# Kernel tuning notes

Measured on AMD Instinct MI355X. Metric: run time of the kernel, lower is better.

Reference implementation:

```python
import jax, jax.numpy as jnp
import numpy as np

N = 100000      # spots (nodes)
E = 1600000     # directed edges
D_IN = 1000     # genes
ALPHA = 0.9
BN_EPS = 1e-3   # BatchNorm(momentum=0.01, eps=0.001), eval mode


def _bn(x, g, b, m, v):
    # eval-mode batchnorm with running stats
    return (x - m) * jax.lax.rsqrt(v + BN_EPS) * g + b


def _gcn(h, row, col, w, b):
    # PyG GCNConv: h' = D^-1/2 (A + I) D^-1/2 (h W) + b
    n = h.shape[0]
    h = h @ w
    ones = jnp.ones((row.shape[0],), h.dtype)
    deg = jnp.ones((n,), h.dtype).at[col].add(ones)  # degree incl. self-loop
    dinv = jax.lax.rsqrt(deg)
    msg = h[row] * (dinv[row] * dinv[col])[:, None]   # gather + edge norm
    agg = jnp.zeros_like(h).at[col].add(msg)          # scatter-add
    agg = agg + h * (1.0 / deg)[:, None]              # self-loop term
    return agg + b


def setup_inputs() -> dict:
    key = jax.random.key(0)
    ks = iter(jax.random.split(key, 48))
    f32 = jnp.float32

    def glorot(shape):
        return jax.random.normal(next(ks), shape, f32) * np.float32(1.0 / np.sqrt(shape[0]))

    def bnp(n):
        g = jax.random.uniform(next(ks), (n,), f32, 0.9, 1.1)
        b = jax.random.normal(next(ks), (n,), f32) * 0.1
        m = jax.random.normal(next(ks), (n,), f32) * 0.1
        v = jax.random.uniform(next(ks), (n,), f32, 0.5, 1.5)
        return g, b, m, v

    inp = {}
    inp['x'] = jax.random.normal(next(ks), (N, D_IN), f32)
    inp['edge_index'] = jax.random.randint(next(ks), (2, E), 0, N, jnp.int64)
    # encoder L0: 1000 -> 256
    inp['enc0_w'] = glorot((D_IN, 256)); inp['enc0_b'] = jnp.zeros((256,), f32)
    inp['enc0_g'], inp['enc0_bb'], inp['enc0_m'], inp['enc0_v'] = bnp(256)
    # encoder L1: 256 -> 64
    inp['enc1_w'] = glorot((256, 64)); inp['enc1_b'] = jnp.zeros((64,), f32)
    inp['enc1_g'], inp['enc1_bb'], inp['enc1_m'], inp['enc1_v'] = bnp(64)
    # GCN: 64 -> 128 (conv_hidden[0]*2)
    inp['conv_w'] = glorot((64, 128)); inp['conv_b'] = jnp.zeros((128,), f32)
    inp['conv_g'], inp['conv_bb'], inp['conv_m'], inp['conv_v'] = bnp(128)
    # GCN mean / logvar heads: 128 -> 16
    inp['mean_w'] = glorot((128, 16)); inp['mean_b'] = jnp.zeros((16,), f32)
    inp['logvar_w'] = glorot((128, 16)); inp['logvar_b'] = jnp.zeros((16,), f32)
    # decoder L0: 80 -> 64
    inp['dec0_w'] = glorot((80, 64)); inp['dec0_b'] = jnp.zeros((64,), f32)
    inp['dec0_g'], inp['dec0_bb'], inp['dec0_m'], inp['dec0_v'] = bnp(64)
    # decoder L1: 64 -> 1000
    inp['dec1_w'] = glorot((64, D_IN)); inp['dec1_b'] = jnp.zeros((D_IN,), f32)
    # cluster layer [15, 80]
    inp['cluster'] = jax.random.normal(next(ks), (15, 80), f32) * np.float32(np.sqrt(2.0 / (15 + 80)))
    return inp


def reference(x, edge_index, enc0_w, enc0_b, enc0_g, enc0_bb, enc0_m, enc0_v,
              enc1_w, enc1_b, enc1_g, enc1_bb, enc1_m, enc1_v,
              conv_w, conv_b, conv_g, conv_bb, conv_m, conv_v,
              mean_w, mean_b, logvar_w, logvar_b,
              dec0_w, dec0_b, dec0_g, dec0_bb, dec0_m, dec0_v,
              dec1_w, dec1_b, cluster):
    row, col = edge_index[0], edge_index[1]
    # linear encoder (Linear + BN(eval) + ELU; dropout off in eval)
    h = jax.nn.elu(_bn(x @ enc0_w + enc0_b, enc0_g, enc0_bb, enc0_m, enc0_v))
    feat_x = jax.nn.elu(_bn(h @ enc1_w + enc1_b, enc1_g, enc1_bb, enc1_m, enc1_v))
    # graph encoder
    c = jax.nn.relu(_bn(_gcn(feat_x, row, col, conv_w, conv_b), conv_g, conv_bb, conv_m, conv_v))
    mu = _gcn(c, row, col, mean_w, mean_b)
    logvar = _gcn(c, row, col, logvar_w, logvar_b)
    gnn_z = mu  # reparameterize in eval mode returns mu
    z = jnp.concatenate([feat_x, gnn_z], axis=1)  # [N, 80]
    # decoder
    d = jax.nn.elu(_bn(z @ dec0_w + dec0_b, dec0_g, dec0_bb, dec0_m, dec0_v))
    de_feat = d @ dec1_w + dec1_b
    # student-t cluster soft assignment (||z-c||^2 via expansion, no [N,K,80] tensor)
    dist = jnp.maximum(jnp.sum(z * z, 1, keepdims=True)
                       + jnp.sum(cluster * cluster, 1)[None, :]
                       - 2.0 * (z @ cluster.T), 0.0)
    q = 1.0 / (1.0 + dist / ALPHA + 1e-8)
    q = q ** ((ALPHA + 1.0) / 2.0)
    q = q / jnp.sum(q, 1, keepdims=True)
    return (z, mu, logvar, de_feat, q, feat_x, gnn_z)
```

## Files before the change

### kernel.cpp

```cpp
#include <hip/hip_runtime.h>
#include <hip/hip_bf16.h>

#define NN 100000
#define NE 1600000
#define DIN 1000
#define BN_EPS 1e-3f
#define NB 391

#define OZ  ((size_t)0)
#define OMU ((size_t)NN*80)
#define OLV ((size_t)NN*96)
#define ODE ((size_t)NN*112)
#define OQ  ((size_t)NN*1112)
#define OFX ((size_t)NN*1127)
#define OGZ ((size_t)NN*1191)

typedef __attribute__((ext_vector_type(8))) short short8v;
typedef __attribute__((ext_vector_type(4))) short short4v;
typedef __attribute__((ext_vector_type(4))) float f32x4;

__device__ __forceinline__ float elu_f(float x) { return x > 0.f ? x : expf(x) - 1.f; }

__device__ __forceinline__ short f2bf(float f) {
    union { float f; unsigned u; } c; c.f = f;
    unsigned r = c.u + 0x7fffu + ((c.u >> 16) & 1u);
    return (short)(r >> 16);
}
__device__ __forceinline__ float b2f(short s) {
    union { unsigned u; float f; } c; c.u = ((unsigned)(unsigned short)s) << 16; return c.f;
}
__device__ __forceinline__ float b2f_lo(unsigned p) {
    union { unsigned u; float f; } c; c.u = p << 16; return c.f;
}
__device__ __forceinline__ float b2f_hi(unsigned p) {
    union { unsigned u; float f; } c; c.u = p & 0xffff0000u; return c.f;
}

__device__ __forceinline__ int edge_at(const void* ei, int is64, size_t idx) {
    if (is64) return (int)((const long long*)ei)[idx];
    return ((const int*)ei)[idx];
}

__global__ __launch_bounds__(256) void k_deg_init(const int* __restrict__ ei,
                                                  float* __restrict__ deg, int* __restrict__ flag) {
    const int i = blockIdx.x * 256 + threadIdx.x;
    if (i < NN) deg[i] = 1.0f;
    if (blockIdx.x == 0) {
        __shared__ int nz;
        if (threadIdx.x == 0) nz = 0;
        __syncthreads();
        for (int j = threadIdx.x; j < 2048; j += 256)
            if (ei[2 * j + 1] != 0) nz = 1;
        __syncthreads();
        if (threadIdx.x == 0) flag[0] = (nz == 0) ? 1 : 0;
    }
}

__global__ __launch_bounds__(256) void k_deg_accum(const void* __restrict__ ei, const int* __restrict__ flag,
                                                   float* __restrict__ deg) {
    const int is64 = flag[0];
    int e = blockIdx.x * 256 + threadIdx.x;
    if (e < NE) atomicAdd(&deg[edge_at(ei, is64, (size_t)NE + e)], 1.0f);
}

__global__ __launch_bounds__(256) void k_scan1(const float* __restrict__ deg, int* __restrict__ off,
                                               int* __restrict__ bsum, int* __restrict__ cursor) {
    __shared__ int s[256];
    const int t = threadIdx.x;
    const int i = blockIdx.x * 256 + t;
    const int vv = (i < NN) ? ((int)deg[i]) - 1 : 0;
    if (i < NN) cursor[i] = 0;
    s[t] = vv;
    __syncthreads();
    for (int d = 1; d < 256; d <<= 1) {
        const int u = (t >= d) ? s[t - d] : 0;
        __syncthreads();
        s[t] += u;
        __syncthreads();
    }
    if (i < NN) off[i] = s[t] - vv;
    if (t == 255) bsum[blockIdx.x] = s[t];
}

__global__ __launch_bounds__(512) void k_scan2(int* __restrict__ bsum) {
    __shared__ int s[512];
    const int t = threadIdx.x;
    const int vv = (t < NB) ? bsum[t] : 0;
    s[t] = vv;
    __syncthreads();
    for (int d = 1; d < 512; d <<= 1) {
        const int u = (t >= d) ? s[t - d] : 0;
        __syncthreads();
        s[t] += u;
        __syncthreads();
    }
    if (t < NB) bsum[t] = s[t] - vv;
}

__global__ __launch_bounds__(256) void k_scan3(int* __restrict__ off, const int* __restrict__ bsum) {
    const int i = blockIdx.x * 256 + threadIdx.x;
    if (i < NN) off[i] += bsum[blockIdx.x];
}

__global__ __launch_bounds__(256) void k_fill(const void* __restrict__ ei, const int* __restrict__ flag,
                                              const float* __restrict__ deg, const int* __restrict__ off,
                                              int* __restrict__ cursor, int2* __restrict__ csr_e) {
    const int is64 = flag[0];
    const int e = blockIdx.x * 256 + threadIdx.x;
    if (e >= NE) return;
    const int r = edge_at(ei, is64, e);
    const int c = edge_at(ei, is64, (size_t)NE + e);
    const float w = rsqrtf(deg[r]) * rsqrtf(deg[c]);
    const int p = atomicAdd(&cursor[c], 1);
    csr_e[off[c] + p] = make_int2(r, __float_as_int(w));
}

__global__ __launch_bounds__(256) void k_wts(const float* __restrict__ w0, short* __restrict__ wt,
                                             const float* __restrict__ w1, short* __restrict__ wt2) {
    const int bid = blockIdx.x;
    if (bid < 1024) {
        const int tid = bid * 256 + threadIdx.x;
        const int c = tid >> 10;
        const int k = tid & 1023;
        wt[((size_t)(k >> 3) * 256 + c) * 8 + (k & 7)] = (k < DIN) ? f2bf(w0[(size_t)k * 256 + c]) : (short)0;
    } else {
        const int tid = (bid - 1024) * 256 + threadIdx.x;
        const int c = tid >> 6;
        const int k = tid & 63;
        wt2[(size_t)c * 64 + k] = (c < DIN) ? f2bf(w1[(size_t)k * DIN + c]) : (short)0;
    }
}

__global__ __launch_bounds__(512, 2) void k_enc0_mfma(
    const float* __restrict__ x, const short* __restrict__ wt, const float* __restrict__ bias,
    const float* __restrict__ g, const float* __restrict__ bb,
    const float* __restrict__ m, const float* __restrict__ v,
    short* __restrict__ h1bf)
{
    __shared__ short smem[24576];
    const int t = threadIdx.x;
    const int lane = t & 63;
    const int wave = t >> 6;
    const int wm = (wave >> 2) * 64;
    const int wn = (wave & 3) * 64;
    const int row0 = blockIdx.x * 128;

    f32x4 acc[4][4];
    #pragma unroll
    for (int mi = 0; mi < 4; ++mi)
        #pragma unroll
        for (int ni = 0; ni < 4; ++ni)
            acc[mi][ni] = (f32x4){0.f, 0.f, 0.f, 0.f};

    const int kq = t & 7;
    const int rA0 = t >> 3;
    const int rA1 = rA0 + 64;
    const int gr0 = (row0 + rA0 < NN) ? (row0 + rA0) : (NN - 1);
    const int gr1 = (row0 + rA1 < NN) ? (row0 + rA1) : (NN - 1);
    const float* xb0 = x + (size_t)gr0 * DIN;
    const float* xb1 = x + (size_t)gr1 * DIN;
    const size_t aoff0 = (((kq >> 1) * 128) + rA0) * 8 + (kq & 1) * 4;
    const size_t aoff1 = (((kq >> 1) * 128) + rA1) * 8 + (kq & 1) * 4;

    const int colB = t & 255;
    const int kcB0 = t >> 8;
    const int kcB1 = 2 + (t >> 8);
    const size_t boff0 = ((size_t)kcB0 * 256 + colB) * 8;
    const size_t boff1 = ((size_t)kcB1 * 256 + colB) * 8;

    const int kc = lane >> 4;
    const int lr = lane & 15;

    {
        const float4 f0 = *reinterpret_cast<const float4*>(xb0 + kq * 4);
        const float4 f1 = *reinterpret_cast<const float4*>(xb1 + kq * 4);
        short4v p0, p1;
        p0[0] = f2bf(f0.x); p0[1] = f2bf(f0.y); p0[2] = f2bf(f0.z); p0[3] = f2bf(f0.w);
        p1[0] = f2bf(f1.x); p1[1] = f2bf(f1.y); p1[2] = f2bf(f1.z); p1[3] = f2bf(f1.w);
        *reinterpret_cast<short4v*>(&smem[aoff0]) = p0;
        *reinterpret_cast<short4v*>(&smem[aoff1]) = p1;
        *reinterpret_cast<short8v*>(&smem[8192 + boff0]) =
            *reinterpret_cast<const short8v*>(&wt[((size_t)kcB0 * 256 + colB) * 8]);
        *reinterpret_cast<short8v*>(&smem[8192 + boff1]) =
            *reinterpret_cast<const short8v*>(&wt[((size_t)kcB1 * 256 + colB) * 8]);
    }
    __syncthreads();

    for (int ks = 0; ks < 32; ++ks) {
        const int cur = ks & 1;
        const int nxt = cur ^ 1;
        const int abase_c = cur * 4096;
        const int bbase_c = 8192 + cur * 8192;
        float4 pf0, pf1;
        short8v wb0, wb1;
        const bool have_next = (ks + 1) < 32;
        bool next_a_ok = false;
        if (have_next) {
            const int kb2 = (ks + 1) * 32 + kq * 4;
            next_a_ok = (kb2 + 4 <= DIN);
            const int ko = next_a_ok ? kb2 : 0;
            pf0 = *reinterpret_cast<const float4*>(xb0 + ko);
            pf1 = *reinterpret_cast<const float4*>(xb1 + ko);
            const int gbase = (ks + 1) * 4;
            wb0 = *reinterpret_cast<const short8v*>(&wt[((size_t)(gbase + kcB0) * 256 + colB) * 8]);
            wb1 = *reinterpret_cast<const short8v*>(&wt[((size_t)(gbase + kcB1) * 256 + colB) * 8]);
        }
        short8v a[4], b[4];
        #pragma unroll
        for (int mi = 0; mi < 4; ++mi)
            a[mi] = *reinterpret_cast<const short8v*>(&smem[abase_c + ((size_t)kc * 128 + wm + mi * 16 + lr) * 8]);
        #pragma unroll
        for (int ni = 0; ni < 4; ++ni)
            b[ni] = *reinterpret_cast<const short8v*>(&smem[bbase_c + ((size_t)kc * 256 + wn + ni * 16 + lr) * 8]);
        #pragma unroll
        for (int mi = 0; mi < 4; ++mi)
            #pragma unroll
            for (int ni = 0; ni < 4; ++ni)
                acc[mi][ni] = __builtin_amdgcn_mfma_f32_16x16x32_bf16(a[mi], b[ni], acc[mi][ni], 0, 0, 0);
        if (have_next) {
            const int abase_n = nxt * 4096;
            const int bbase_n = 8192 + nxt * 8192;
            short4v p0, p1;
            if (next_a_ok) {
                p0[0] = f2bf(pf0.x); p0[1] = f2bf(pf0.y); p0[2] = f2bf(pf0.z); p0[3] = f2bf(pf0.w);
                p1[0] = f2bf(pf1.x); p1[1] = f2bf(pf1.y); p1[2] = f2bf(pf1.z); p1[3] = f2bf(pf1.w);
            } else {
                p0 = (short4v){0, 0, 0, 0};
                p1 = (short4v){0, 0, 0, 0};
            }
            *reinterpret_cast<short4v*>(&smem[abase_n + aoff0]) = p0;
            *reinterpret_cast<short4v*>(&smem[abase_n + aoff1]) = p1;
            *reinterpret_cast<short8v*>(&smem[bbase_n + boff0]) = wb0;
            *reinterpret_cast<short8v*>(&smem[bbase_n + boff1]) = wb1;
        }
        __syncthreads();
    }

    float sc[4], sh[4];
    #pragma unroll
    for (int ni = 0; ni < 4; ++ni) {
        const int col = wn + ni * 16 + lr;
        const float s = rsqrtf(v[col] + BN_EPS) * g[col];
        sc[ni] = s;
        sh[ni] = (bias[col] - m[col]) * s + bb[col];
    }
    #pragma unroll
    for (int p = 0; p < 2; ++p) {
        __syncthreads();
        if ((wave >> 2) == p) {
            #pragma unroll
            for (int mi = 0; mi < 4; ++mi) {
                #pragma unroll
                for (int j = 0; j < 4; ++j) {
                    const int lrow = mi * 16 + (lane >> 4) * 4 + j;
                    #pragma unroll
                    for (int ni = 0; ni < 4; ++ni) {
                        const float y = acc[mi][ni][j] * sc[ni] + sh[ni];
                        smem[lrow * 256 + wn + ni * 16 + lr] = f2bf(elu_f(y));
                    }
                }
            }
        }
        __syncthreads();
        for (int idx = t; idx < 2048; idx += 512) {
            const int r = idx >> 5;
            const int c8 = (idx & 31) * 8;
            const int row = row0 + p * 64 + r;
            if (row < NN)
                *reinterpret_cast<short8v*>(&h1bf[(size_t)row * 256 + c8]) =
                    *reinterpret_cast<const short8v*>(&smem[r * 256 + c8]);
        }
    }
}

__global__ __launch_bounds__(256) void k_enc1(
    const short* __restrict__ h1bf, const float* __restrict__ w, const float* __restrict__ bias,
    const float* __restrict__ g, const float* __restrict__ bb,
    const float* __restrict__ m, const float* __restrict__ v,
    float* __restrict__ feat, short* __restrict__ featbf, float* __restrict__ out)
{
    __shared__ short hs[32 * 256];
    const int t = threadIdx.x;
    const int row0 = blockIdx.x * 32;
    const int j0 = t & 31;
    const int r0 = (t >> 5) * 4;
    float acc[4][2] = {};
    for (int idx = t; idx < 1024; idx += 256) {
        const int r = idx >> 5, c8 = idx & 31;
        *reinterpret_cast<short8v*>(&hs[r * 256 + c8 * 8]) =
            *reinterpret_cast<const short8v*>(&h1bf[(size_t)(row0 + r) * 256 + c8 * 8]);
    }
    __syncthreads();
    #pragma unroll 1
    for (int k = 0; k < 256; k += 8) {
        float wv[8][2];
        #pragma unroll
        for (int kk = 0; kk < 8; ++kk) {
            wv[kk][0] = w[(k + kk) * 64 + j0];
            wv[kk][1] = w[(k + kk) * 64 + j0 + 32];
        }
        #pragma unroll
        for (int r = 0; r < 4; ++r) {
            const short8v hv = *reinterpret_cast<const short8v*>(&hs[(r0 + r) * 256 + k]);
            #pragma unroll
            for (int kk = 0; kk < 8; ++kk) {
                const float xa = b2f(hv[kk]);
                acc[r][0] = fmaf(xa, wv[kk][0], acc[r][0]);
                acc[r][1] = fmaf(xa, wv[kk][1], acc[r][1]);
            }
        }
    }
    #pragma unroll
    for (int c = 0; c < 2; ++c) {
        const int j = j0 + 32 * c;
        const float sc = rsqrtf(v[j] + BN_EPS) * g[j];
        const float sh = (bias[j] - m[j]) * sc + bb[j];
        #pragma unroll
        for (int r = 0; r < 4; ++r) {
            const size_t rowi = row0 + r0 + r;
            const float y = elu_f(acc[r][c] * sc + sh);
            feat[rowi * 64 + j] = y;
            featbf[rowi * 64 + j] = f2bf(y);
            out[OFX + rowi * 64 + j] = y;
            out[OZ + rowi * 80 + j] = y;
        }
    }
}

__global__ __launch_bounds__(256) void k_feat_gather(
    const unsigned* __restrict__ featp, const float* __restrict__ deg,
    const int* __restrict__ off, const int2* __restrict__ csr_e,
    float* __restrict__ aggF)
{
    const int t = threadIdx.x;
    const int node = blockIdx.x * 8 + (t >> 5);
    const int lane = t & 31;
    const float dg = deg[node];
    const float dinv = 1.0f / dg;
    const unsigned ps = featp[(size_t)node * 32 + lane];
    float a0 = b2f_lo(ps) * dinv;
    float a1 = b2f_hi(ps) * dinv;
    const int beg = off[node];
    const int end = beg + ((int)dg - 1);
    for (int s = beg; s < end; ++s) {
        const int2 e = csr_e[s];
        const float w = __int_as_float(e.y);
        const unsigned p = featp[(size_t)e.x * 32 + lane];
        a0 = fmaf(b2f_lo(p), w, a0);
        a1 = fmaf(b2f_hi(p), w, a1);
    }
    float2 o; o.x = a0; o.y = a1;
    *reinterpret_cast<float2*>(&aggF[(size_t)node * 64 + lane * 2]) = o;
}

__global__ __launch_bounds__(256) void k_conv_mlp_proj(
    const float* __restrict__ aggF, const float* __restrict__ w, const float* __restrict__ cb,
    const float* __restrict__ g, const float* __restrict__ bb,
    const float* __restrict__ m, const float* __restrict__ v,
    const float* __restrict__ mw, const float* __restrict__ lw,
    short* __restrict__ m2bf)
{
    __shared__ float fs[32 * 64];
    __shared__ float cs[32 * 128];
    const int t = threadIdx.x;
    const int row0 = blockIdx.x * 32;
    {
        const int j0 = t & 63;
        const int r0 = (t >> 6) * 8;
        float acc[8][2] = {};
        for (int idx = t; idx < 512; idx += 256) {
            const int r = idx >> 4, c4 = idx & 15;
            *reinterpret_cast<float4*>(&fs[r * 64 + c4 * 4]) =
                *reinterpret_cast<const float4*>(&aggF[(size_t)(row0 + r) * 64 + c4 * 4]);
        }
        __syncthreads();
        #pragma unroll 1
        for (int k = 0; k < 64; k += 4) {
            float wv[4][2];
            #pragma unroll
            for (int kk = 0; kk < 4; ++kk) {
                wv[kk][0] = w[(k + kk) * 128 + j0];
                wv[kk][1] = w[(k + kk) * 128 + j0 + 64];
            }
            #pragma unroll
            for (int r = 0; r < 8; ++r) {
                const float4 xv = *reinterpret_cast<const float4*>(&fs[(r0 + r) * 64 + k]);
                const float xa[4] = {xv.x, xv.y, xv.z, xv.w};
                #pragma unroll
                for (int kk = 0; kk < 4; ++kk) {
                    acc[r][0] = fmaf(xa[kk], wv[kk][0], acc[r][0]);
                    acc[r][1] = fmaf(xa[kk], wv[kk][1], acc[r][1]);
                }
            }
        }
        #pragma unroll
        for (int c = 0; c < 2; ++c) {
            const int j = j0 + 64 * c;
            const float sc = rsqrtf(v[j] + BN_EPS) * g[j];
            const float sh = bb[j] - m[j] * sc;
            const float cbj = cb[j];
            #pragma unroll
            for (int r = 0; r < 8; ++r) {
                const float val = acc[r][c] + cbj;
                cs[(r0 + r) * 128 + j] = fmaxf(fmaf(val, sc, sh), 0.f);
            }
        }
    }
    __syncthreads();
    {
        const int j0 = t & 15;
        const int r0 = (t >> 4) * 2;
        float acc[2][2] = {};
        #pragma unroll 1
        for (int k = 0; k < 128; k += 4) {
            float wv[4][2];
            #pragma unroll
            for (int kk = 0; kk < 4; ++kk) {
                wv[kk][0] = mw[(k + kk) * 16 + j0];
                wv[kk][1] = lw[(k + kk) * 16 + j0];
            }
            #pragma unroll
            for (int r = 0; r < 2; ++r) {
                const float4 xv = *reinterpret_cast<const float4*>(&cs[(r0 + r) * 128 + k]);
                const float xa[4] = {xv.x, xv.y, xv.z, xv.w};
                #pragma unroll
                for (int kk = 0; kk < 4; ++kk) {
                    acc[r][0] = fmaf(xa[kk], wv[kk][0], acc[r][0]);
                    acc[r][1] = fmaf(xa[kk], wv[kk][1], acc[r][1]);
                }
            }
        }
        #pragma unroll
        for (int r = 0; r < 2; ++r) {
            const size_t rowi = row0 + r0 + r;
            m2bf[rowi * 32 + j0] = f2bf(acc[r][0]);
            m2bf[rowi * 32 + 16 + j0] = f2bf(acc[r][1]);
        }
    }
}

__global__ __launch_bounds__(256) void k_mlp_gather(
    const unsigned* __restrict__ m2p, const float* __restrict__ deg,
    const int* __restrict__ off, const int2* __restrict__ csr_e,
    const float* __restrict__ mb, const float* __restrict__ lb,
    float* __restrict__ agg2)
{
    const int t = threadIdx.x;
    const int node = blockIdx.x * 16 + (t >> 4);
    const int lane = t & 15;
    const int f0 = lane * 2, f1 = lane * 2 + 1;
    const float dg = deg[node];
    const float dinv = 1.0f / dg;
    const float b0 = (f0 < 16) ? mb[f0] : lb[f0 - 16];
    const float b1 = (f1 < 16) ? mb[f1] : lb[f1 - 16];
    const unsigned ps = m2p[(size_t)node * 16 + lane];
    float a0 = fmaf(b2f_lo(ps), dinv, b0);
    float a1 = fmaf(b2f_hi(ps), dinv, b1);
    const int beg = off[node];
    const int end = beg + ((int)dg - 1);
    for (int s = beg; s < end; ++s) {
        const int2 e = csr_e[s];
        const float w = __int_as_float(e.y);
        const unsigned p = m2p[(size_t)e.x * 16 + lane];
        a0 = fmaf(b2f_lo(p), w, a0);
        a1 = fmaf(b2f_hi(p), w, a1);
    }
    float2 o; o.x = a0; o.y = a1;
    *reinterpret_cast<float2*>(&agg2[(size_t)node * 32 + lane * 2]) = o;
}

__global__ __launch_bounds__(256) void k_final_pre(
    const float* __restrict__ feat, const float* __restrict__ agg2,
    const float* __restrict__ d0w, const float* __restrict__ d0b,
    const float* __restrict__ g, const float* __restrict__ bb,
    const float* __restrict__ m, const float* __restrict__ v,
    const float* __restrict__ cluster,
    short* __restrict__ d0bf,
    float* __restrict__ out)
{
    __shared__ float zs[8][80];
    __shared__ float qs[8][15];
    const int t = threadIdx.x;
    const int row0 = blockIdx.x * 8;

    for (int idx = t; idx < 512; idx += 256) {
        const int r = idx >> 6, k = idx & 63;
        zs[r][k] = feat[(size_t)(row0 + r) * 64 + k];
    }
    if (t < 128) {
        const int r = t >> 4, k = t & 15;
        const size_t rowi = row0 + r;
        const float muv = agg2[rowi * 32 + k];
        const float lv = agg2[rowi * 32 + 16 + k];
        zs[r][64 + k] = muv;
        out[OMU + rowi * 16 + k] = muv;
        out[OGZ + rowi * 16 + k] = muv;
        out[OZ + rowi * 80 + 64 + k] = muv;
        out[OLV + rowi * 16 + k] = lv;
    }
    __syncthreads();

    for (int idx = t; idx < 512; idx += 256) {
        const int r = idx >> 6, n = idx & 63;
        float acc = 0.f;
        #pragma unroll
        for (int k = 0; k < 80; k += 4) {
            const float4 zv = *reinterpret_cast<const float4*>(&zs[r][k]);
            acc = fmaf(zv.x, d0w[(k + 0) * 64 + n], acc);
            acc = fmaf(zv.y, d0w[(k + 1) * 64 + n], acc);
            acc = fmaf(zv.z, d0w[(k + 2) * 64 + n], acc);
            acc = fmaf(zv.w, d0w[(k + 3) * 64 + n], acc);
        }
        acc += d0b[n];
        const float sc = rsqrtf(v[n] + BN_EPS) * g[n];
        const float y = elu_f((acc - m[n]) * sc + bb[n]);
        d0bf[(size_t)(row0 + r) * 64 + n] = f2bf(y);
    }

    if (t < 120) {
        const int r = t / 15, c = t % 15;
        float zz = 0.f, cc = 0.f, dot = 0.f;
        #pragma unroll 1
        for (int k = 0; k < 80; ++k) {
            const float zv = zs[r][k];
            const float cv = cluster[c * 80 + k];
            zz = fmaf(zv, zv, zz);
            cc = fmaf(cv, cv, cc);
            dot = fmaf(zv, cv, dot);
        }
        const float dist = fmaxf(zz + cc - 2.f * dot, 0.f);
        qs[r][c] = powf(1.0f / (1.0f + dist / 0.9f + 1e-8f), 0.95f);
    }
    __syncthreads();
    if (t < 120) {
        const int r = t / 15, c = t % 15;
        float s = 0.f;
        #pragma unroll
        for (int c2 = 0; c2 < 15; ++c2) s += qs[r][c2];
        out[OQ + (size_t)(row0 + r) * 15 + c] = qs[r][c] / s;
    }
}

__global__ __launch_bounds__(256) void k_dec1_mfma(
    const short* __restrict__ d0bf, const short* __restrict__ wt2,
    const float* __restrict__ d1b, float* __restrict__ out)
{
    __shared__ float ots[128 * 128];
    const int t = threadIdx.x;
    const int lane = t & 63;
    const int wave = t >> 6;
    const int wm = (wave >> 1) * 64;
    const int wn = (wave & 1) * 64;
    const int row0 = blockIdx.x * 128;
    const int col0 = blockIdx.y * 128;
    const int kc = lane >> 4;
    const int lr = lane & 15;

    f32x4 acc[4][4];
    #pragma unroll
    for (int mi = 0; mi < 4; ++mi)
        #pragma unroll
        for (int ni = 0; ni < 4; ++ni)
            acc[mi][ni] = (f32x4){0.f, 0.f, 0.f, 0.f};

    #pragma unroll
    for (int ks = 0; ks < 2; ++ks) {
        const int k0 = ks * 32 + kc * 8;
        short8v a[4], b[4];
        #pragma unroll
        for (int mi = 0; mi < 4; ++mi) {
            const int row = row0 + wm + mi * 16 + lr;
            if (row < NN)
                a[mi] = *reinterpret_cast<const short8v*>(&d0bf[(size_t)row * 64 + k0]);
            else
                a[mi] = (short8v){0, 0, 0, 0, 0, 0, 0, 0};
        }
        #pragma unroll
        for (int ni = 0; ni < 4; ++ni) {
            const int col = col0 + wn + ni * 16 + lr;
            b[ni] = *reinterpret_cast<const short8v*>(&wt2[(size_t)col * 64 + k0]);
        }
        #pragma unroll
        for (int mi = 0; mi < 4; ++mi)
            #pragma unroll
            for (int ni = 0; ni < 4; ++ni)
                acc[mi][ni] = __builtin_amdgcn_mfma_f32_16x16x32_bf16(a[mi], b[ni], acc[mi][ni], 0, 0, 0);
    }

    #pragma unroll
    for (int ni = 0; ni < 4; ++ni) {
        const int lcol = wn + ni * 16 + lr;
        const int gcol = col0 + lcol;
        const float bv = d1b[(gcol < DIN) ? gcol : (DIN - 1)];
        #pragma unroll
        for (int mi = 0; mi < 4; ++mi) {
            #pragma unroll
            for (int j = 0; j < 4; ++j) {
                const int lrow = wm + mi * 16 + (lane >> 4) * 4 + j;
                ots[lrow * 128 + lcol] = acc[mi][ni][j] + bv;
            }
        }
    }
    __syncthreads();

    for (int idx = t; idx < 128 * 32; idx += 256) {
        const int r = idx >> 5;
        const int c4 = (idx & 31) * 4;
        const int row = row0 + r;
        const int col = col0 + c4;
        if (row < NN && col < DIN) {
            const float4 val = *reinterpret_cast<const float4*>(&ots[r * 128 + c4]);
            *reinterpret_cast<float4*>(&out[ODE + (size_t)row * DIN + col]) = val;
        }
    }
}

extern "C" void kernel_launch(void* const* d_in, const int* in_sizes, int n_in,
                              void* d_out, int out_size, void* d_ws, size_t ws_size,
                              hipStream_t stream)
{
    const float* x       = (const float*)d_in[0];
    const void*  ei      = d_in[1];
    const float* enc0_w  = (const float*)d_in[2];
    const float* enc0_b  = (const float*)d_in[3];
    const float* enc0_g  = (const float*)d_in[4];
    const float* enc0_bb = (const float*)d_in[5];
    const float* enc0_m  = (const float*)d_in[6];
    const float* enc0_v  = (const float*)d_in[7];
    const float* enc1_w  = (const float*)d_in[8];
    const float* enc1_b  = (const float*)d_in[9];
    const float* enc1_g  = (const float*)d_in[10];
    const float* enc1_bb = (const float*)d_in[11];
    const float* enc1_m  = (const float*)d_in[12];
    const float* enc1_v  = (const float*)d_in[13];
    const float* conv_w  = (const float*)d_in[14];
    const float* conv_b  = (const float*)d_in[15];
    const float* conv_g  = (const float*)d_in[16];
    const float* conv_bb = (const float*)d_in[17];
    const float* conv_m  = (const float*)d_in[18];
    const float* conv_v  = (const float*)d_in[19];
    const float* mean_w  = (const float*)d_in[20];
    const float* mean_b  = (const float*)d_in[21];
    const float* logvar_w = (const float*)d_in[22];
    const float* logvar_b = (const float*)d_in[23];
    const float* dec0_w  = (const float*)d_in[24];
    const float* dec0_b  = (const float*)d_in[25];
    const float* dec0_g  = (const float*)d_in[26];
    const float* dec0_bb = (const float*)d_in[27];
    const float* dec0_m  = (const float*)d_in[28];
    const float* dec0_v  = (const float*)d_in[29];
    const float* dec1_w  = (const float*)d_in[30];
    const float* dec1_b  = (const float*)d_in[31];
    const float* cluster = (const float*)d_in[32];

    float* ws = (float*)d_ws;
    float* deg  = ws;
    float* feat = ws + NN;
    float* A    = ws + (size_t)65 * NN;
    size_t base = (size_t)321 * NN;
    int*   off     = (int*)(ws + base);
    int*   cursor  = (int*)(ws + base + NN);
    int*   bsum    = (int*)(ws + base + 2 * (size_t)NN);
    int2*  csr_e   = (int2*)(ws + base + 2 * (size_t)NN + 512);
    short* wt      = (short*)(ws + base + 2 * (size_t)NN + 512 + 2 * (size_t)NE);
    short* wt2     = wt + 262144;
    int*   flag    = (int*)(ws + base + 2 * (size_t)NN + 512 + 2 * (size_t)NE + 131072 + 32768);

    short* h1bf   = (short*)A;
    short* featbf = (short*)(A + (size_t)128 * NN);
    float* aggF   = A;
    short* m2bf   = (short*)(A + (size_t)128 * NN);
    float* agg2   = A + (size_t)32 * NN;
    short* d0bf   = (short*)(A + (size_t)64 * NN);

    float* out = (float*)d_out;

    k_deg_init<<<NB, 256, 0, stream>>>((const int*)ei, deg, flag);
    k_deg_accum<<<NE / 256, 256, 0, stream>>>(ei, flag, deg);

    k_scan1<<<NB, 256, 0, stream>>>(deg, off, bsum, cursor);
    k_scan2<<<1, 512, 0, stream>>>(bsum);
    k_scan3<<<NB, 256, 0, stream>>>(off, bsum);
    k_fill<<<NE / 256, 256, 0, stream>>>(ei, flag, deg, off, cursor, csr_e);

    k_wts<<<1280, 256, 0, stream>>>(enc0_w, wt, dec1_w, wt2);
    k_enc0_mfma<<<(NN + 127) / 128, 512, 0, stream>>>(x, wt, enc0_b, enc0_g, enc0_bb, enc0_m, enc0_v, h1bf);

    k_enc1<<<NN / 32, 256, 0, stream>>>(h1bf, enc1_w, enc1_b, enc1_g, enc1_bb, enc1_m, enc1_v,
                                        feat, featbf, out);

    k_feat_gather<<<NN / 8, 256, 0, stream>>>((const unsigned*)featbf, deg, off, csr_e, aggF);
    k_conv_mlp_proj<<<NN / 32, 256, 0, stream>>>(aggF, conv_w, conv_b,
                                                 conv_g, conv_bb, conv_m, conv_v,
                                                 mean_w, logvar_w, m2bf);

    k_mlp_gather<<<NN / 16, 256, 0, stream>>>((const unsigned*)m2bf, deg, off, csr_e,
                                              mean_b, logvar_b, agg2);

    k_final_pre<<<NN / 8, 256, 0, stream>>>(feat, agg2, dec0_w, dec0_b, dec0_g, dec0_bb, dec0_m, dec0_v,
                                            cluster, d0bf, out);
    {
        dim3 grid((NN + 127) / 128, 8);
        k_dec1_mfma<<<grid, 256, 0, stream>>>(d0bf, wt2, dec1_b, out);
    }
}
```

Measured before the change: 969.4 us.

## Factor GCN edge normalization into source/destination scaling and unroll gathers

Instead of storing a per-edge weight dinv[r]*dinv[c] in the CSR, source features are pre-scaled by rsqrt(deg) when written in bf16 and the gathered sum is scaled by the destination's rsqrt(deg). The CSR shrinks from int2 to int, which halves edge-list traffic, and the fill kernel no longer reads deg. The gather loops are unrolled by four with independent accumulators so more loads are in flight. Scaling before bf16 rounding slightly changes numerics, and the self-loop term now comes out as rsq*rsq*h, equal to h/deg.

Result: faster. 903.8 us (median of 2 runs) (-6.8%).

```diff
diff --git a/kernel.cpp b/kernel.cpp
--- a/kernel.cpp
+++ b/kernel.cpp
@@ -103,16 +103,15 @@
 }
 
 __global__ __launch_bounds__(256) void k_fill(const void* __restrict__ ei, const int* __restrict__ flag,
-                                              const float* __restrict__ deg, const int* __restrict__ off,
-                                              int* __restrict__ cursor, int2* __restrict__ csr_e) {
+                                              const int* __restrict__ off,
+                                              int* __restrict__ cursor, int* __restrict__ csr_src) {
     const int is64 = flag[0];
     const int e = blockIdx.x * 256 + threadIdx.x;
     if (e >= NE) return;
     const int r = edge_at(ei, is64, e);
     const int c = edge_at(ei, is64, (size_t)NE + e);
-    const float w = rsqrtf(deg[r]) * rsqrtf(deg[c]);
     const int p = atomicAdd(&cursor[c], 1);
-    csr_e[off[c] + p] = make_int2(r, __float_as_int(w));
+    csr_src[off[c] + p] = r;
 }
 
 __global__ __launch_bounds__(256) void k_wts(const float* __restrict__ w0, short* __restrict__ wt,
@@ -277,6 +276,7 @@
     const short* __restrict__ h1bf, const float* __restrict__ w, const float* __restrict__ bias,
     const float* __restrict__ g, const float* __restrict__ bb,
     const float* __restrict__ m, const float* __restrict__ v,
+    const float* __restrict__ deg,
     float* __restrict__ feat, short* __restrict__ featbf, float* __restrict__ out)
 {
     __shared__ short hs[32 * 256];
@@ -319,8 +319,9 @@
         for (int r = 0; r < 4; ++r) {
             const size_t rowi = row0 + r0 + r;
             const float y = elu_f(acc[r][c] * sc + sh);
+            const float rsq = rsqrtf(deg[rowi]);
             feat[rowi * 64 + j] = y;
-            featbf[rowi * 64 + j] = f2bf(y);
+            featbf[rowi * 64 + j] = f2bf(y * rsq);
             out[OFX + rowi * 64 + j] = y;
             out[OZ + rowi * 80 + j] = y;
         }
@@ -329,27 +330,37 @@
 
 __global__ __launch_bounds__(256) void k_feat_gather(
     const unsigned* __restrict__ featp, const float* __restrict__ deg,
-    const int* __restrict__ off, const int2* __restrict__ csr_e,
+    const int* __restrict__ off, const int* __restrict__ csr_src,
     float* __restrict__ aggF)
 {
     const int t = threadIdx.x;
     const int node = blockIdx.x * 8 + (t >> 5);
     const int lane = t & 31;
-    const float dg = deg[node];
-    const float dinv = 1.0f / dg;
+    const float rsq = rsqrtf(deg[node]);
     const unsigned ps = featp[(size_t)node * 32 + lane];
-    float a0 = b2f_lo(ps) * dinv;
-    float a1 = b2f_hi(ps) * dinv;
+    float ax = b2f_lo(ps), ay = b2f_hi(ps);
+    float bx = 0.f, by = 0.f, cx = 0.f, cy = 0.f, dx = 0.f, dy = 0.f;
     const int beg = off[node];
-    const int end = beg + ((int)dg - 1);
-    for (int s = beg; s < end; ++s) {
-        const int2 e = csr_e[s];
-        const float w = __int_as_float(e.y);
-        const unsigned p = featp[(size_t)e.x * 32 + lane];
-        a0 = fmaf(b2f_lo(p), w, a0);
-        a1 = fmaf(b2f_hi(p), w, a1);
-    }
-    float2 o; o.x = a0; o.y = a1;
+    const int end = beg + ((int)deg[node] - 1);
+    int s = beg;
+    for (; s + 4 <= end; s += 4) {
+        const int r0 = csr_src[s], r1 = csr_src[s + 1], r2 = csr_src[s + 2], r3 = csr_src[s + 3];
+        const unsigned p0 = featp[(size_t)r0 * 32 + lane];
+        const unsigned p1 = featp[(size_t)r1 * 32 + lane];
+        const unsigned p2 = featp[(size_t)r2 * 32 + lane];
+        const unsigned p3 = featp[(size_t)r3 * 32 + lane];
+        ax += b2f_lo(p0); ay += b2f_hi(p0);
+        bx += b2f_lo(p1); by += b2f_hi(p1);
+        cx += b2f_lo(p2); cy += b2f_hi(p2);
+        dx += b2f_lo(p3); dy += b2f_hi(p3);
+    }
+    for (; s < end; ++s) {
+        const unsigned p0 = featp[(size_t)csr_src[s] * 32 + lane];
+        ax += b2f_lo(p0); ay += b2f_hi(p0);
+    }
+    float2 o;
+    o.x = rsq * ((ax + bx) + (cx + dx));
+    o.y = rsq * ((ay + by) + (cy + dy));
     *reinterpret_cast<float2*>(&aggF[(size_t)node * 64 + lane * 2]) = o;
 }
 
@@ -358,6 +369,7 @@
     const float* __restrict__ g, const float* __restrict__ bb,
     const float* __restrict__ m, const float* __restrict__ v,
     const float* __restrict__ mw, const float* __restrict__ lw,
+    const float* __restrict__ deg,
     short* __restrict__ m2bf)
 {
     __shared__ float fs[32 * 64];
@@ -433,15 +445,16 @@
         #pragma unroll
         for (int r = 0; r < 2; ++r) {
             const size_t rowi = row0 + r0 + r;
-            m2bf[rowi * 32 + j0] = f2bf(acc[r][0]);
-            m2bf[rowi * 32 + 16 + j0] = f2bf(acc[r][1]);
+            const float rsq = rsqrtf(deg[rowi]);
+            m2bf[rowi * 32 + j0] = f2bf(acc[r][0] * rsq);
+            m2bf[rowi * 32 + 16 + j0] = f2bf(acc[r][1] * rsq);
         }
     }
 }
 
 __global__ __launch_bounds__(256) void k_mlp_gather(
     const unsigned* __restrict__ m2p, const float* __restrict__ deg,
-    const int* __restrict__ off, const int2* __restrict__ csr_e,
+    const int* __restrict__ off, const int* __restrict__ csr_src,
     const float* __restrict__ mb, const float* __restrict__ lb,
     float* __restrict__ agg2)
 {
@@ -449,23 +462,33 @@
     const int node = blockIdx.x * 16 + (t >> 4);
     const int lane = t & 15;
     const int f0 = lane * 2, f1 = lane * 2 + 1;
-    const float dg = deg[node];
-    const float dinv = 1.0f / dg;
+    const float rsq = rsqrtf(deg[node]);
     const float b0 = (f0 < 16) ? mb[f0] : lb[f0 - 16];
     const float b1 = (f1 < 16) ? mb[f1] : lb[f1 - 16];
     const unsigned ps = m2p[(size_t)node * 16 + lane];
-    float a0 = fmaf(b2f_lo(ps), dinv, b0);
-    float a1 = fmaf(b2f_hi(ps), dinv, b1);
+    float ax = b2f_lo(ps), ay = b2f_hi(ps);
+    float bx = 0.f, by = 0.f, cx = 0.f, cy = 0.f, dx = 0.f, dy = 0.f;
     const int beg = off[node];
-    const int end = beg + ((int)dg - 1);
-    for (int s = beg; s < end; ++s) {
-        const int2 e = csr_e[s];
-        const float w = __int_as_float(e.y);
-        const unsigned p = m2p[(size_t)e.x * 16 + lane];
-        a0 = fmaf(b2f_lo(p), w, a0);
-        a1 = fmaf(b2f_hi(p), w, a1);
-    }
-    float2 o; o.x = a0; o.y = a1;
+    const int end = beg + ((int)deg[node] - 1);
+    int s = beg;
+    for (; s + 4 <= end; s += 4) {
+        const int r0 = csr_src[s], r1 = csr_src[s + 1], r2 = csr_src[s + 2], r3 = csr_src[s + 3];
+        const unsigned p0 = m2p[(size_t)r0 * 16 + lane];
+        const unsigned p1 = m2p[(size_t)r1 * 16 + lane];
+        const unsigned p2 = m2p[(size_t)r2 * 16 + lane];
+        const unsigned p3 = m2p[(size_t)r3 * 16 + lane];
+        ax += b2f_lo(p0); ay += b2f_hi(p0);
+        bx += b2f_lo(p1); by += b2f_hi(p1);
+        cx += b2f_lo(p2); cy += b2f_hi(p2);
+        dx += b2f_lo(p3); dy += b2f_hi(p3);
+    }
+    for (; s < end; ++s) {
+        const unsigned p0 = m2p[(size_t)csr_src[s] * 16 + lane];
+        ax += b2f_lo(p0); ay += b2f_hi(p0);
+    }
+    float2 o;
+    o.x = fmaf(rsq, (ax + bx) + (cx + dx), b0);
+    o.y = fmaf(rsq, (ay + by) + (cy + dy), b1);
     *reinterpret_cast<float2*>(&agg2[(size_t)node * 32 + lane * 2]) = o;
 }
 
@@ -661,7 +684,7 @@
     int*   off     = (int*)(ws + base);
     int*   cursor  = (int*)(ws + base + NN);
     int*   bsum    = (int*)(ws + base + 2 * (size_t)NN);
-    int2*  csr_e   = (int2*)(ws + base + 2 * (size_t)NN + 512);
+    int*   csr_src = (int*)(ws + base + 2 * (size_t)NN + 512);
     short* wt      = (short*)(ws + base + 2 * (size_t)NN + 512 + 2 * (size_t)NE);
     short* wt2     = wt + 262144;
     int*   flag    = (int*)(ws + base + 2 * (size_t)NN + 512 + 2 * (size_t)NE + 131072 + 32768);
@@ -681,20 +704,20 @@
     k_scan1<<<NB, 256, 0, stream>>>(deg, off, bsum, cursor);
     k_scan2<<<1, 512, 0, stream>>>(bsum);
     k_scan3<<<NB, 256, 0, stream>>>(off, bsum);
-    k_fill<<<NE / 256, 256, 0, stream>>>(ei, flag, deg, off, cursor, csr_e);
+    k_fill<<<NE / 256, 256, 0, stream>>>(ei, flag, off, cursor, csr_src);
 
     k_wts<<<1280, 256, 0, stream>>>(enc0_w, wt, dec1_w, wt2);
     k_enc0_mfma<<<(NN + 127) / 128, 512, 0, stream>>>(x, wt, enc0_b, enc0_g, enc0_bb, enc0_m, enc0_v, h1bf);
 
-    k_enc1<<<NN / 32, 256, 0, stream>>>(h1bf, enc1_w, enc1_b, enc1_g, enc1_bb, enc1_m, enc1_v,
+    k_enc1<<<NN / 32, 256, 0, stream>>>(h1bf, enc1_w, enc1_b, enc1_g, enc1_bb, enc1_m, enc1_v, deg,
                                         feat, featbf, out);
 
-    k_feat_gather<<<NN / 8, 256, 0, stream>>>((const unsigned*)featbf, deg, off, csr_e, aggF);
+    k_feat_gather<<<NN / 8, 256, 0, stream>>>((const unsigned*)featbf, deg, off, csr_src, aggF);
     k_conv_mlp_proj<<<NN / 32, 256, 0, stream>>>(aggF, conv_w, conv_b,
                                                  conv_g, conv_bb, conv_m, conv_v,
-                                                 mean_w, logvar_w, m2bf);
-
-    k_mlp_gather<<<NN / 16, 256, 0, stream>>>((const unsigned*)m2bf, deg, off, csr_e,
+                                                 mean_w, logvar_w, deg, m2bf);
+
+    k_mlp_gather<<<NN / 16, 256, 0, stream>>>((const unsigned*)m2bf, deg, off, csr_src,
                                               mean_b, logvar_b, agg2);
 
     k_final_pre<<<NN / 8, 256, 0, stream>>>(feat, agg2, dec0_w, dec0_b, dec0_g, dec0_bb, dec0_m, dec0_v,
```
